# Kernel optimization log

Hardware: AMD Instinct MI355X
Metric: run time of the kernel (lower is better)

Reference implementation:

```python
import jax, jax.numpy as jnp
import numpy as np

B, D, N, H = 4, 1024, 2048, 16
HD = D // H  # head dim = 64


def rotate_half(x):
    # pairs (x1, x2) -> (-x2, x1), interleaved along last dim
    x1 = x[..., 0::2]
    x2 = x[..., 1::2]
    return jnp.stack((-x2, x1), axis=-1).reshape(x.shape)


def apply_cached_rotary_emb(freqs, t):
    return t * freqs[0] + rotate_half(t) * freqs[1]


def setup_inputs() -> dict:
    key = jax.random.key(0)
    ks = jax.random.split(key, 13)
    s = 1.0 / np.sqrt(D)
    inp = {
        "query": jax.random.normal(ks[0], (B, D, N), jnp.float32),
        "key": jax.random.normal(ks[1], (B, D, N), jnp.float32),
        "value": jax.random.normal(ks[2], (B, D, N), jnp.float32),
        "encoding": jax.random.normal(ks[3], (2, 1, 1, N, HD), jnp.float32),
        "Wq": jax.random.normal(ks[4], (D, D), jnp.float32) * s,
        "bq": jax.random.normal(ks[5], (D,), jnp.float32) * s,
        "Wk": jax.random.normal(ks[6], (D, D), jnp.float32) * s,
        "bk": jax.random.normal(ks[7], (D,), jnp.float32) * s,
        "Wv": jax.random.normal(ks[8], (D, D), jnp.float32) * s,
        "bv": jax.random.normal(ks[9], (D,), jnp.float32) * s,
        "Wm": jax.random.normal(ks[10], (D, D), jnp.float32) * s,
        "bm": jax.random.normal(ks[11], (D,), jnp.float32) * s,
    }
    return inp


def reference(query, key, value, encoding, Wq, bq, Wk, bk, Wv, bv, Wm, bm):
    b, d_model, n = query.shape

    def proj(W, bias, x):  # Conv1d with kernel_size=1 == pointwise matmul
        return jnp.einsum('oi,bin->bon', W, x) + bias[None, :, None]

    # [B, D, N] -> [B, HD, H, N]  (channel split: dim-major, as in .view(B, dim, H, -1))
    q = proj(Wq, bq, query).reshape(b, HD, H, n)
    k = proj(Wk, bk, key).reshape(b, HD, H, n)
    v = proj(Wv, bv, value).reshape(b, HD, H, n)

    # RoPE applied in [B, H, N, HD] layout, then back to [B, HD, H, N]
    q = jnp.transpose(apply_cached_rotary_emb(encoding, jnp.transpose(q, (0, 2, 3, 1))), (0, 3, 1, 2))
    k = jnp.transpose(apply_cached_rotary_emb(encoding, jnp.transpose(k, (0, 2, 3, 1))), (0, 3, 1, 2))

    scores = jnp.einsum('bdhn,bdhm->bhnm', q, k) / np.float32(np.sqrt(HD))
    prob = jax.nn.softmax(scores, axis=-1)
    x = jnp.einsum('bhnm,bdhm->bdhn', prob, v)

    out = jnp.einsum('oi,bin->bon', Wm, x.reshape(b, d_model, n)) + bm[None, :, None]
    return out
```

## Files before the change

kernel.cpp:

```cpp
#include <hip/hip_runtime.h>
#include <hip/hip_bf16.h>

typedef __bf16 bf16;
typedef __bf16 bf16x8 __attribute__((ext_vector_type(8)));
typedef __bf16 bf16x4 __attribute__((ext_vector_type(4)));
typedef float f32x4 __attribute__((ext_vector_type(4)));

#define LOG2E 1.44269504088896340736f

typedef __attribute__((address_space(1))) const unsigned int guint;
typedef __attribute__((address_space(3))) unsigned int luint;

__device__ __forceinline__ void gload_lds16(const bf16* g, bf16* l) {
  __builtin_amdgcn_global_load_lds((guint*)g, (luint*)l, 16, 0, 0);
}

__global__ __launch_bounds__(256) void k_transpose3(const float* __restrict__ q,
                                                    const float* __restrict__ k,
                                                    const float* __restrict__ v,
                                                    bf16* __restrict__ tq,
                                                    bf16* __restrict__ tk,
                                                    bf16* __restrict__ tv) {
  __shared__ bf16 T[64][72];
  const int t = threadIdx.x;
  const int n0 = blockIdx.x * 64;
  const int i0 = blockIdx.y * 64;
  const int z = blockIdx.z;
  const int b = z & 3, which = z >> 2;
  const float* src = (which == 0) ? q : ((which == 1) ? k : v);
  bf16* dst = (which == 0) ? tq : ((which == 1) ? tk : tv);
  const size_t srcb = (size_t)b * 1024 * 2048;
#pragma unroll
  for (int p = 0; p < 2; ++p) {
    int idx = p * 256 + t;
    int row = idx >> 3;
    int seg = idx & 7;
    const float* sp = src + srcb + (size_t)(i0 + row) * 2048 + n0 + seg * 8;
    f32x4 a = *(const f32x4*)sp;
    f32x4 c = *(const f32x4*)(sp + 4);
    bf16x8 o;
#pragma unroll
    for (int e = 0; e < 4; ++e) { o[e] = (bf16)a[e]; o[4 + e] = (bf16)c[e]; }
    *(bf16x8*)&T[row][seg * 8] = o;
  }
  __syncthreads();
  const int j = t >> 2;
  const int iseg = t & 3;
  bf16x8 o0, o1;
#pragma unroll
  for (int e = 0; e < 8; ++e) o0[e] = T[iseg * 16 + e][j];
#pragma unroll
  for (int e = 0; e < 8; ++e) o1[e] = T[iseg * 16 + 8 + e][j];
  bf16* dp = dst + (size_t)b * 2048 * 1024 + (size_t)(n0 + j) * 1024 + i0 + iseg * 16;
  *(bf16x8*)dp = o0;
  *(bf16x8*)(dp + 8) = o1;
}

__global__ __launch_bounds__(256) void k_gemm3(const bf16* __restrict__ Wqb,
                                               const bf16* __restrict__ Wkb,
                                               const bf16* __restrict__ Wvb,
                                               const float* __restrict__ bq,
                                               const float* __restrict__ bk,
                                               const float* __restrict__ bv,
                                               const bf16* __restrict__ tq,
                                               const bf16* __restrict__ tk,
                                               const bf16* __restrict__ tv,
                                               bf16* __restrict__ qp,
                                               bf16* __restrict__ kp,
                                               bf16* __restrict__ vp) {
  const int K = 1024, Nn = 2048;
  const int z = blockIdx.z;
  const int b = z & 3, which = z >> 2;
  const bf16* A = (which == 0) ? Wqb : ((which == 1) ? Wkb : Wvb);
  const bf16* Bt = (which == 0) ? tq : ((which == 1) ? tk : tv);
  const float* bias = (which == 0) ? bq : ((which == 1) ? bk : bv);
  bf16* C = (which == 0) ? qp : ((which == 1) ? kp : vp);

  __shared__ bf16 As[128 * 32];
  __shared__ bf16 Bs[128 * 32];
  const int t = threadIdx.x;
  const int w = t >> 6, l = t & 63, q = l >> 4, li = l & 15;
  const int o0 = blockIdx.y * 128, n0 = blockIdx.x * 128;
  const bf16* Ab = A + (size_t)o0 * K;
  const bf16* Bb = Bt + (size_t)b * Nn * K + (size_t)n0 * K;
  const int wr = (w >> 1) * 64, wc = (w & 1) * 64;
  f32x4 acc[4][4];
#pragma unroll
  for (int i = 0; i < 4; ++i)
#pragma unroll
    for (int j = 0; j < 4; ++j) acc[i][j] = (f32x4){0.f, 0.f, 0.f, 0.f};

  const int sidx0 = w * 64 + l;
  const int srow0 = sidx0 >> 2, sseg0 = (sidx0 & 3) * 8;
  const int sidx1 = 256 + sidx0;
  const int srow1 = sidx1 >> 2, sseg1 = (sidx1 & 3) * 8;
  bf16* ldsA0 = As + (size_t)(w * 64) * 8;
  bf16* ldsA1 = As + (size_t)(256 + w * 64) * 8;
  bf16* ldsB0 = Bs + (size_t)(w * 64) * 8;
  bf16* ldsB1 = Bs + (size_t)(256 + w * 64) * 8;

  for (int k0 = 0; k0 < K; k0 += 32) {
    __syncthreads();
    gload_lds16(Ab + (size_t)srow0 * K + k0 + sseg0, ldsA0);
    gload_lds16(Ab + (size_t)srow1 * K + k0 + sseg1, ldsA1);
    gload_lds16(Bb + (size_t)srow0 * K + k0 + sseg0, ldsB0);
    gload_lds16(Bb + (size_t)srow1 * K + k0 + sseg1, ldsB1);
    __syncthreads();
    bf16x8 af[4], bfr[4];
#pragma unroll
    for (int mt = 0; mt < 4; ++mt) af[mt] = *(const bf16x8*)&As[(wr + mt * 16 + li) * 32 + q * 8];
#pragma unroll
    for (int c = 0; c < 4; ++c) bfr[c] = *(const bf16x8*)&Bs[(wc + c * 16 + li) * 32 + q * 8];
#pragma unroll
    for (int mt = 0; mt < 4; ++mt)
#pragma unroll
      for (int c = 0; c < 4; ++c)
        acc[mt][c] = __builtin_amdgcn_mfma_f32_16x16x32_bf16(af[mt], bfr[c], acc[mt][c], 0, 0, 0);
  }

  bf16* Cb = C + (size_t)b * K * Nn;
#pragma unroll
  for (int mt = 0; mt < 4; ++mt) {
#pragma unroll
    for (int r = 0; r < 4; ++r) {
      int o = o0 + wr + mt * 16 + q * 4 + r;
      float bvv = bias[o];
#pragma unroll
      for (int c = 0; c < 4; ++c) {
        int n = n0 + wc + c * 16 + li;
        Cb[(size_t)o * Nn + n] = (bf16)(acc[mt][c][r] + bvv);
      }
    }
  }
}

template <typename OT>
__global__ __launch_bounds__(256) void k_gemm(const bf16* __restrict__ A,
                                              const bf16* __restrict__ Bt,
                                              const float* __restrict__ bias,
                                              OT* __restrict__ C,
                                              int M, int K, int Nn) {
  __shared__ bf16 As[128 * 32];
  __shared__ bf16 Bs[128 * 32];
  const int t = threadIdx.x;
  const int w = t >> 6, l = t & 63, q = l >> 4, li = l & 15;
  const int o0 = blockIdx.y * 128, n0 = blockIdx.x * 128;
  const int b = blockIdx.z;
  const bf16* Ab = A + (size_t)o0 * K;
  const bf16* Bb = Bt + (size_t)b * Nn * K + (size_t)n0 * K;
  const int wr = (w >> 1) * 64, wc = (w & 1) * 64;
  f32x4 acc[4][4];
#pragma unroll
  for (int i = 0; i < 4; ++i)
#pragma unroll
    for (int j = 0; j < 4; ++j) acc[i][j] = (f32x4){0.f, 0.f, 0.f, 0.f};

  const int sidx0 = w * 64 + l;
  const int srow0 = sidx0 >> 2, sseg0 = (sidx0 & 3) * 8;
  const int sidx1 = 256 + sidx0;
  const int srow1 = sidx1 >> 2, sseg1 = (sidx1 & 3) * 8;
  bf16* ldsA0 = As + (size_t)(w * 64) * 8;
  bf16* ldsA1 = As + (size_t)(256 + w * 64) * 8;
  bf16* ldsB0 = Bs + (size_t)(w * 64) * 8;
  bf16* ldsB1 = Bs + (size_t)(256 + w * 64) * 8;

  for (int k0 = 0; k0 < K; k0 += 32) {
    __syncthreads();
    gload_lds16(Ab + (size_t)srow0 * K + k0 + sseg0, ldsA0);
    gload_lds16(Ab + (size_t)srow1 * K + k0 + sseg1, ldsA1);
    gload_lds16(Bb + (size_t)srow0 * K + k0 + sseg0, ldsB0);
    gload_lds16(Bb + (size_t)srow1 * K + k0 + sseg1, ldsB1);
    __syncthreads();
    bf16x8 af[4], bfr[4];
#pragma unroll
    for (int mt = 0; mt < 4; ++mt) af[mt] = *(const bf16x8*)&As[(wr + mt * 16 + li) * 32 + q * 8];
#pragma unroll
    for (int c = 0; c < 4; ++c) bfr[c] = *(const bf16x8*)&Bs[(wc + c * 16 + li) * 32 + q * 8];
#pragma unroll
    for (int mt = 0; mt < 4; ++mt)
#pragma unroll
      for (int c = 0; c < 4; ++c)
        acc[mt][c] = __builtin_amdgcn_mfma_f32_16x16x32_bf16(af[mt], bfr[c], acc[mt][c], 0, 0, 0);
  }

  OT* Cb = C + (size_t)b * M * Nn;
#pragma unroll
  for (int mt = 0; mt < 4; ++mt) {
#pragma unroll
    for (int r = 0; r < 4; ++r) {
      int o = o0 + wr + mt * 16 + q * 4 + r;
      float bv = bias[o];
#pragma unroll
      for (int c = 0; c < 4; ++c) {
        int n = n0 + wc + c * 16 + li;
        Cb[(size_t)o * Nn + n] = (OT)(acc[mt][c][r] + bv);
      }
    }
  }
}

__global__ __launch_bounds__(256) void k_rope2(const bf16* __restrict__ qp,
                                               const bf16* __restrict__ kp,
                                               const float* __restrict__ enc,
                                               bf16* __restrict__ qa,
                                               bf16* __restrict__ ka) {
  __shared__ bf16 T[64][72];
  const int t = threadIdx.x;
  const int n0 = blockIdx.x * 64;
  const int h = blockIdx.y;
  const int z = blockIdx.z;
  const int b = z & 3, which = z >> 2;
  const bf16* src = which ? kp : qp;
  bf16* dst = which ? ka : qa;
  const float oscale = which ? 1.0f : 0.125f * LOG2E;
#pragma unroll
  for (int p = 0; p < 2; ++p) {
    int idx = p * 256 + t;
    int hd = idx >> 3;
    int seg = idx & 7;
    *(bf16x8*)&T[hd][seg * 8] =
        *(const bf16x8*)(src + (size_t)(b * 1024 + hd * 16 + h) * 2048 + n0 + seg * 8);
  }
  __syncthreads();
  const int j = t >> 2;
  const int hd0 = (t & 3) * 16;
  const int n = n0 + j;
  const float* e0 = enc + (size_t)n * 64 + hd0;
  const float* e1 = enc + (size_t)2048 * 64 + (size_t)n * 64 + hd0;
  bf16x8 o0, o1;
#pragma unroll
  for (int i = 0; i < 8; ++i) {
    int e = 2 * i;
    float t0 = (float)T[hd0 + e][j];
    float t1 = (float)T[hd0 + e + 1][j];
    float f00 = e0[e], f01 = e0[e + 1];
    float f10 = e1[e], f11 = e1[e + 1];
    float r0 = (t0 * f00 - t1 * f10) * oscale;
    float r1 = (t1 * f01 + t0 * f11) * oscale;
    if (i < 4) { o0[e & 7] = (bf16)r0; o0[(e & 7) + 1] = (bf16)r1; }
    else       { o1[e & 7] = (bf16)r0; o1[(e & 7) + 1] = (bf16)r1; }
  }
  bf16* dp = dst + ((size_t)(b * 16 + h) * 2048 + n) * 64 + hd0;
  *(bf16x8*)dp = o0;
  *(bf16x8*)(dp + 8) = o1;
}

__global__ __launch_bounds__(256, 4) void k_attn(const bf16* __restrict__ qa,
                                                 const bf16* __restrict__ ka,
                                                 const bf16* __restrict__ vp,
                                                 bf16* __restrict__ xo) {
  __shared__ bf16 Ks[64 * 72];
  __shared__ bf16 Vs[64 * 72];
  __shared__ bf16 Ps[4][32 * 72];
  const int t = threadIdx.x;
  const int w = t >> 6, l = t & 63, q = l >> 4, li = l & 15;
  const int n0 = blockIdx.x * 128, h = blockIdx.y, b = blockIdx.z;
  const bf16* Qb = qa + (size_t)(b * 16 + h) * 2048 * 64;
  const bf16* Kb = ka + (size_t)(b * 16 + h) * 2048 * 64;
  const bf16* Vb = vp + (size_t)b * 1024 * 2048 + (size_t)h * 2048;
  bf16* Pw = &Ps[w][0];

  const int r0 = t >> 3, s0 = (t & 7) * 8;
  const int r1 = (256 + t) >> 3, s1 = (t & 7) * 8;

  bf16x8 qf[2][2];
#pragma unroll
  for (int bt = 0; bt < 2; ++bt)
#pragma unroll
    for (int kk = 0; kk < 2; ++kk)
      qf[bt][kk] = *(const bf16x8*)(Qb + (size_t)(n0 + w * 32 + bt * 16 + li) * 64 + kk * 32 + q * 8);

  bf16x8 onef;
#pragma unroll
  for (int e = 0; e < 8; ++e) onef[e] = (bf16)1.0f;

  f32x4 acc[4][2];
#pragma unroll
  for (int i = 0; i < 4; ++i)
#pragma unroll
    for (int j = 0; j < 2; ++j) acc[i][j] = (f32x4){0.f, 0.f, 0.f, 0.f};
  f32x4 accl[2] = {(f32x4){0.f, 0.f, 0.f, 0.f}, (f32x4){0.f, 0.f, 0.f, 0.f}};

  bf16x8 kr0, kr1, vr0, vr1;
  kr0 = *(const bf16x8*)(Kb + (size_t)r0 * 64 + s0);
  kr1 = *(const bf16x8*)(Kb + (size_t)r1 * 64 + s1);
  vr0 = *(const bf16x8*)(Vb + (size_t)r0 * 32768 + s0);
  vr1 = *(const bf16x8*)(Vb + (size_t)r1 * 32768 + s1);
  *(bf16x8*)&Ks[r0 * 72 + s0] = kr0;
  *(bf16x8*)&Ks[r1 * 72 + s1] = kr1;
  *(bf16x8*)&Vs[r0 * 72 + s0] = vr0;
  *(bf16x8*)&Vs[r1 * 72 + s1] = vr1;
  __syncthreads();

  for (int m0 = 0; m0 < 2048; m0 += 64) {
    const int mn = (m0 + 64 < 2048) ? m0 + 64 : m0;
    kr0 = *(const bf16x8*)(Kb + (size_t)(mn + r0) * 64 + s0);
    kr1 = *(const bf16x8*)(Kb + (size_t)(mn + r1) * 64 + s1);
    vr0 = *(const bf16x8*)(Vb + (size_t)r0 * 32768 + mn + s0);
    vr1 = *(const bf16x8*)(Vb + (size_t)r1 * 32768 + mn + s1);

    f32x4 sacc[4][2];
#pragma unroll
    for (int mt = 0; mt < 4; ++mt)
#pragma unroll
      for (int bt = 0; bt < 2; ++bt) sacc[mt][bt] = (f32x4){0.f, 0.f, 0.f, 0.f};
#pragma unroll
    for (int kk = 0; kk < 2; ++kk) {
#pragma unroll
      for (int mt = 0; mt < 4; ++mt) {
        bf16x8 af = *(const bf16x8*)&Ks[(mt * 16 + li) * 72 + kk * 32 + q * 8];
#pragma unroll
        for (int bt = 0; bt < 2; ++bt)
          sacc[mt][bt] = __builtin_amdgcn_mfma_f32_16x16x32_bf16(af, qf[bt][kk], sacc[mt][bt], 0, 0, 0);
      }
    }

#pragma unroll
    for (int mt = 0; mt < 4; ++mt)
#pragma unroll
      for (int bt = 0; bt < 2; ++bt) {
        bf16x4 pk;
#pragma unroll
        for (int r = 0; r < 4; ++r) pk[r] = (bf16)__builtin_amdgcn_exp2f(sacc[mt][bt][r]);
        *(bf16x4*)&Pw[(bt * 16 + li) * 72 + mt * 16 + q * 4] = pk;
      }
    asm volatile("s_waitcnt lgkmcnt(0)" ::: "memory");

#pragma unroll
    for (int kk = 0; kk < 2; ++kk) {
      bf16x8 pf[2];
#pragma unroll
      for (int bt = 0; bt < 2; ++bt) {
        pf[bt] = *(const bf16x8*)&Pw[(bt * 16 + li) * 72 + kk * 32 + q * 8];
        accl[bt] = __builtin_amdgcn_mfma_f32_16x16x32_bf16(onef, pf[bt], accl[bt], 0, 0, 0);
      }
#pragma unroll
      for (int hdt = 0; hdt < 4; ++hdt) {
        bf16x8 vf = *(const bf16x8*)&Vs[(hdt * 16 + li) * 72 + kk * 32 + q * 8];
#pragma unroll
        for (int bt = 0; bt < 2; ++bt)
          acc[hdt][bt] = __builtin_amdgcn_mfma_f32_16x16x32_bf16(vf, pf[bt], acc[hdt][bt], 0, 0, 0);
      }
    }

    __syncthreads();
    *(bf16x8*)&Ks[r0 * 72 + s0] = kr0;
    *(bf16x8*)&Ks[r1 * 72 + s1] = kr1;
    *(bf16x8*)&Vs[r0 * 72 + s0] = vr0;
    *(bf16x8*)&Vs[r1 * 72 + s1] = vr1;
    __syncthreads();
  }

  float inv[2] = {1.0f / accl[0][0], 1.0f / accl[1][0]};

  bf16* xb = xo + (size_t)b * 2048 * 1024 + (size_t)h * 64;
#pragma unroll
  for (int hdt = 0; hdt < 4; ++hdt)
#pragma unroll
    for (int bt = 0; bt < 2; ++bt) {
      int n = n0 + w * 32 + bt * 16 + li;
      bf16x4 o;
#pragma unroll
      for (int r = 0; r < 4; ++r) o[r] = (bf16)(acc[hdt][bt][r] * inv[bt]);
      *(bf16x4*)(xb + (size_t)n * 1024 + hdt * 16 + q * 4) = o;
    }
}

__global__ __launch_bounds__(256) void k_prepw(const float* __restrict__ Wq,
                                               const float* __restrict__ Wk,
                                               const float* __restrict__ Wv,
                                               const float* __restrict__ Wm,
                                               bf16* __restrict__ oq,
                                               bf16* __restrict__ ok,
                                               bf16* __restrict__ ov,
                                               bf16* __restrict__ om) {
  const int which = blockIdx.y;
  if (which < 3) {
    const float* s = (which == 0) ? Wq : ((which == 1) ? Wk : Wv);
    bf16* d = (which == 0) ? oq : ((which == 1) ? ok : ov);
    int idx = (blockIdx.x * 256 + threadIdx.x) * 4;
    f32x4 a = *(const f32x4*)(s + idx);
    bf16x4 o;
#pragma unroll
    for (int e = 0; e < 4; ++e) o[e] = (bf16)a[e];
    *(bf16x4*)(d + idx) = o;
  } else {
#pragma unroll
    for (int p = 0; p < 4; ++p) {
      int idx = (blockIdx.x * 4 + p) * 256 + threadIdx.x;
      int o = idx >> 10, j = idx & 1023;
      int hd = j & 63, hh = j >> 6;
      om[idx] = (bf16)Wm[((size_t)o << 10) + (size_t)(hd * 16 + hh)];
    }
  }
}

extern "C" void kernel_launch(void* const* d_in, const int* in_sizes, int n_in,
                              void* d_out, int out_size, void* d_ws, size_t ws_size,
                              hipStream_t stream) {
  const float* query = (const float*)d_in[0];
  const float* key   = (const float*)d_in[1];
  const float* value = (const float*)d_in[2];
  const float* enc   = (const float*)d_in[3];
  const float* Wq = (const float*)d_in[4];  const float* bq = (const float*)d_in[5];
  const float* Wk = (const float*)d_in[6];  const float* bk = (const float*)d_in[7];
  const float* Wv = (const float*)d_in[8];  const float* bv = (const float*)d_in[9];
  const float* Wm = (const float*)d_in[10]; const float* bm = (const float*)d_in[11];

  char* ws = (char*)d_ws;
  const size_t SZ = (size_t)4 * 2048 * 1024 * 2;
  const size_t WZ = (size_t)1024 * 1024 * 2;
  bf16* bufA = (bf16*)(ws + 0 * SZ);
  bf16* bufB = (bf16*)(ws + 1 * SZ);
  bf16* bufC = (bf16*)(ws + 2 * SZ);
  bf16* bufD = (bf16*)(ws + 3 * SZ);
  bf16* Wqb  = (bf16*)(ws + 4 * SZ + 0 * WZ);
  bf16* Wkb  = (bf16*)(ws + 4 * SZ + 1 * WZ);
  bf16* Wvb  = (bf16*)(ws + 4 * SZ + 2 * WZ);
  bf16* Wmp  = (bf16*)(ws + 4 * SZ + 3 * WZ);
  bf16* vt   = (bf16*)d_out;
  bf16* vpd  = (bf16*)d_out + (size_t)4 * 2048 * 1024;

  dim3 blk(256);
  k_prepw<<<dim3(1024, 4), blk, 0, stream>>>(Wq, Wk, Wv, Wm, Wqb, Wkb, Wvb, Wmp);
  k_transpose3<<<dim3(32, 16, 12), blk, 0, stream>>>(query, key, value, bufA, bufB, vt);
  k_gemm3<<<dim3(16, 8, 12), blk, 0, stream>>>(Wqb, Wkb, Wvb, bq, bk, bv,
                                               bufA, bufB, vt, bufC, bufD, vpd);
  k_rope2<<<dim3(32, 16, 8), blk, 0, stream>>>(bufC, bufD, enc, bufA, bufB);
  k_attn<<<dim3(16, 16, 4), blk, 0, stream>>>(bufA, bufB, vpd, bufC);
  k_gemm<float><<<dim3(16, 8, 4), blk, 0, stream>>>(Wmp, bufC, bm, (float*)d_out, 1024, 1024, 2048);
}
```

Measured before the change: 368.3 us.

## Double-buffer attention K/V tiles, keep P in registers, swizzle transpose LDS

The attention kernel now double-buffers its K/V shared-memory tiles, which drops one barrier per 64-key step. It also rebuilds the P operand for the PV MFMA in registers using permlane32_swap and ds_swizzle, instead of writing P to shared memory and reading it back. The transpose and RoPE kernels XOR-swizzle their LDS tile columns to cut bank conflicts on the column-strided reads. The cost is more LDS for K/V, in-register shuffles that depend on the exact MFMA lane layout, and a correctness risk if the permute mapping is wrong.

After: 378.4 us. 2.7% more time.

```diff
diff --git a/kernel.cpp b/kernel.cpp
--- a/kernel.cpp
+++ b/kernel.cpp
@@ -5,6 +5,8 @@
 typedef __bf16 bf16x8 __attribute__((ext_vector_type(8)));
 typedef __bf16 bf16x4 __attribute__((ext_vector_type(4)));
 typedef float f32x4 __attribute__((ext_vector_type(4)));
+typedef unsigned int uint4v __attribute__((ext_vector_type(4)));
+typedef unsigned int uint2v __attribute__((ext_vector_type(2)));
 
 #define LOG2E 1.44269504088896340736f
 
@@ -35,22 +37,24 @@
     int idx = p * 256 + t;
     int row = idx >> 3;
     int seg = idx & 7;
+    int xm = (row >> 4) << 1;
     const float* sp = src + srcb + (size_t)(i0 + row) * 2048 + n0 + seg * 8;
     f32x4 a = *(const f32x4*)sp;
     f32x4 c = *(const f32x4*)(sp + 4);
     bf16x8 o;
 #pragma unroll
-    for (int e = 0; e < 4; ++e) { o[e] = (bf16)a[e]; o[4 + e] = (bf16)c[e]; }
+    for (int e = 0; e < 4; ++e) { o[e ^ xm] = (bf16)a[e]; o[(4 + e) ^ xm] = (bf16)c[e]; }
     *(bf16x8*)&T[row][seg * 8] = o;
   }
   __syncthreads();
   const int j = t >> 2;
   const int iseg = t & 3;
+  const int jx = j ^ (iseg << 1);
   bf16x8 o0, o1;
 #pragma unroll
-  for (int e = 0; e < 8; ++e) o0[e] = T[iseg * 16 + e][j];
-#pragma unroll
-  for (int e = 0; e < 8; ++e) o1[e] = T[iseg * 16 + 8 + e][j];
+  for (int e = 0; e < 8; ++e) o0[e] = T[iseg * 16 + e][jx];
+#pragma unroll
+  for (int e = 0; e < 8; ++e) o1[e] = T[iseg * 16 + 8 + e][jx];
   bf16* dp = dst + (size_t)b * 2048 * 1024 + (size_t)(n0 + j) * 1024 + i0 + iseg * 16;
   *(bf16x8*)dp = o0;
   *(bf16x8*)(dp + 8) = o1;
@@ -218,12 +222,17 @@
     int idx = p * 256 + t;
     int hd = idx >> 3;
     int seg = idx & 7;
-    *(bf16x8*)&T[hd][seg * 8] =
-        *(const bf16x8*)(src + (size_t)(b * 1024 + hd * 16 + h) * 2048 + n0 + seg * 8);
+    int xm = (hd >> 4) << 1;
+    bf16x8 v = *(const bf16x8*)(src + (size_t)(b * 1024 + hd * 16 + h) * 2048 + n0 + seg * 8);
+    bf16x8 o;
+#pragma unroll
+    for (int e = 0; e < 8; ++e) o[e ^ xm] = v[e];
+    *(bf16x8*)&T[hd][seg * 8] = o;
   }
   __syncthreads();
   const int j = t >> 2;
   const int hd0 = (t & 3) * 16;
+  const int jx = j ^ ((t & 3) << 1);
   const int n = n0 + j;
   const float* e0 = enc + (size_t)n * 64 + hd0;
   const float* e1 = enc + (size_t)2048 * 64 + (size_t)n * 64 + hd0;
@@ -231,8 +240,8 @@
 #pragma unroll
   for (int i = 0; i < 8; ++i) {
     int e = 2 * i;
-    float t0 = (float)T[hd0 + e][j];
-    float t1 = (float)T[hd0 + e + 1][j];
+    float t0 = (float)T[hd0 + e][jx];
+    float t1 = (float)T[hd0 + e + 1][jx];
     float f00 = e0[e], f01 = e0[e + 1];
     float f10 = e1[e], f11 = e1[e + 1];
     float r0 = (t0 * f00 - t1 * f10) * oscale;
@@ -245,20 +254,70 @@
   *(bf16x8*)(dp + 8) = o1;
 }
 
+#define ATTN_COMPUTE(KS, VS)                                                              \
+  {                                                                                       \
+    f32x4 sacc[4][2];                                                                     \
+    _Pragma("unroll") for (int mt = 0; mt < 4; ++mt)                                      \
+        _Pragma("unroll") for (int bt = 0; bt < 2; ++bt)                                  \
+            sacc[mt][bt] = (f32x4){0.f, 0.f, 0.f, 0.f};                                   \
+    _Pragma("unroll") for (int kk = 0; kk < 2; ++kk) {                                    \
+      _Pragma("unroll") for (int mt = 0; mt < 4; ++mt) {                                  \
+        bf16x8 af = *(const bf16x8*)&(KS)[(mt * 16 + li) * 72 + kk * 32 + q * 8];         \
+        _Pragma("unroll") for (int bt = 0; bt < 2; ++bt)                                  \
+            sacc[mt][bt] =                                                                \
+                __builtin_amdgcn_mfma_f32_16x16x32_bf16(af, qf[bt][kk], sacc[mt][bt], 0, 0, 0); \
+      }                                                                                   \
+    }                                                                                     \
+    unsigned pk32[2][4][2];                                                               \
+    _Pragma("unroll") for (int mt = 0; mt < 4; ++mt)                                      \
+        _Pragma("unroll") for (int bt = 0; bt < 2; ++bt) {                                \
+      bf16x4 pk;                                                                          \
+      _Pragma("unroll") for (int r = 0; r < 4; ++r)                                       \
+          pk[r] = (bf16)__builtin_amdgcn_exp2f(sacc[mt][bt][r]);                          \
+      uint2v pu = __builtin_bit_cast(uint2v, pk);                                         \
+      pk32[bt][mt][0] = pu[0];                                                            \
+      pk32[bt][mt][1] = pu[1];                                                            \
+    }                                                                                     \
+    _Pragma("unroll") for (int kk = 0; kk < 2; ++kk) {                                    \
+      bf16x8 pf[2];                                                                       \
+      _Pragma("unroll") for (int bt = 0; bt < 2; ++bt) {                                  \
+        uint4v du;                                                                        \
+        _Pragma("unroll") for (int hh = 0; hh < 2; ++hh) {                                \
+          unsigned p0 = pk32[bt][2 * kk + 0][hh];                                         \
+          unsigned p1 = pk32[bt][2 * kk + 1][hh];                                         \
+          uint2v ab = __builtin_amdgcn_permlane32_swap(p0, p1, false, false);             \
+          unsigned A = ab[0];                                                             \
+          unsigned Bv = ab[1];                                                            \
+          unsigned swzA = (unsigned)__builtin_amdgcn_ds_swizzle((int)A, 0x401F);          \
+          unsigned swzB = (unsigned)__builtin_amdgcn_ds_swizzle((int)Bv, 0x401F);         \
+          du[hh] = oddrow ? swzB : A;                                                     \
+          du[2 + hh] = oddrow ? Bv : swzA;                                                \
+        }                                                                                 \
+        pf[bt] = __builtin_bit_cast(bf16x8, du);                                          \
+        accl[bt] = __builtin_amdgcn_mfma_f32_16x16x32_bf16(onef, pf[bt], accl[bt], 0, 0, 0); \
+      }                                                                                   \
+      _Pragma("unroll") for (int hdt = 0; hdt < 4; ++hdt) {                               \
+        bf16x8 vf = *(const bf16x8*)&(VS)[(hdt * 16 + li) * 72 + kk * 32 + q * 8];        \
+        _Pragma("unroll") for (int bt = 0; bt < 2; ++bt)                                  \
+            acc[hdt][bt] =                                                                \
+                __builtin_amdgcn_mfma_f32_16x16x32_bf16(vf, pf[bt], acc[hdt][bt], 0, 0, 0); \
+      }                                                                                   \
+    }                                                                                     \
+  }
+
 __global__ __launch_bounds__(256, 4) void k_attn(const bf16* __restrict__ qa,
                                                  const bf16* __restrict__ ka,
                                                  const bf16* __restrict__ vp,
                                                  bf16* __restrict__ xo) {
-  __shared__ bf16 Ks[64 * 72];
-  __shared__ bf16 Vs[64 * 72];
-  __shared__ bf16 Ps[4][32 * 72];
+  __shared__ bf16 Ks2[2][64 * 72];
+  __shared__ bf16 Vs2[2][64 * 72];
   const int t = threadIdx.x;
   const int w = t >> 6, l = t & 63, q = l >> 4, li = l & 15;
   const int n0 = blockIdx.x * 128, h = blockIdx.y, b = blockIdx.z;
+  const bool oddrow = ((t >> 4) & 1) != 0;
   const bf16* Qb = qa + (size_t)(b * 16 + h) * 2048 * 64;
   const bf16* Kb = ka + (size_t)(b * 16 + h) * 2048 * 64;
   const bf16* Vb = vp + (size_t)b * 1024 * 2048 + (size_t)h * 2048;
-  bf16* Pw = &Ps[w][0];
 
   const int r0 = t >> 3, s0 = (t & 7) * 8;
   const int r1 = (256 + t) >> 3, s1 = (t & 7) * 8;
@@ -286,69 +345,40 @@
   kr1 = *(const bf16x8*)(Kb + (size_t)r1 * 64 + s1);
   vr0 = *(const bf16x8*)(Vb + (size_t)r0 * 32768 + s0);
   vr1 = *(const bf16x8*)(Vb + (size_t)r1 * 32768 + s1);
-  *(bf16x8*)&Ks[r0 * 72 + s0] = kr0;
-  *(bf16x8*)&Ks[r1 * 72 + s1] = kr1;
-  *(bf16x8*)&Vs[r0 * 72 + s0] = vr0;
-  *(bf16x8*)&Vs[r1 * 72 + s1] = vr1;
+  *(bf16x8*)&Ks2[0][r0 * 72 + s0] = kr0;
+  *(bf16x8*)&Ks2[0][r1 * 72 + s1] = kr1;
+  *(bf16x8*)&Vs2[0][r0 * 72 + s0] = vr0;
+  *(bf16x8*)&Vs2[0][r1 * 72 + s1] = vr1;
   __syncthreads();
 
-  for (int m0 = 0; m0 < 2048; m0 += 64) {
-    const int mn = (m0 + 64 < 2048) ? m0 + 64 : m0;
-    kr0 = *(const bf16x8*)(Kb + (size_t)(mn + r0) * 64 + s0);
-    kr1 = *(const bf16x8*)(Kb + (size_t)(mn + r1) * 64 + s1);
-    vr0 = *(const bf16x8*)(Vb + (size_t)r0 * 32768 + mn + s0);
-    vr1 = *(const bf16x8*)(Vb + (size_t)r1 * 32768 + mn + s1);
-
-    f32x4 sacc[4][2];
-#pragma unroll
-    for (int mt = 0; mt < 4; ++mt)
-#pragma unroll
-      for (int bt = 0; bt < 2; ++bt) sacc[mt][bt] = (f32x4){0.f, 0.f, 0.f, 0.f};
-#pragma unroll
-    for (int kk = 0; kk < 2; ++kk) {
-#pragma unroll
-      for (int mt = 0; mt < 4; ++mt) {
-        bf16x8 af = *(const bf16x8*)&Ks[(mt * 16 + li) * 72 + kk * 32 + q * 8];
-#pragma unroll
-        for (int bt = 0; bt < 2; ++bt)
-          sacc[mt][bt] = __builtin_amdgcn_mfma_f32_16x16x32_bf16(af, qf[bt][kk], sacc[mt][bt], 0, 0, 0);
-      }
-    }
-
-#pragma unroll
-    for (int mt = 0; mt < 4; ++mt)
-#pragma unroll
-      for (int bt = 0; bt < 2; ++bt) {
-        bf16x4 pk;
-#pragma unroll
-        for (int r = 0; r < 4; ++r) pk[r] = (bf16)__builtin_amdgcn_exp2f(sacc[mt][bt][r]);
-        *(bf16x4*)&Pw[(bt * 16 + li) * 72 + mt * 16 + q * 4] = pk;
-      }
-    asm volatile("s_waitcnt lgkmcnt(0)" ::: "memory");
-
-#pragma unroll
-    for (int kk = 0; kk < 2; ++kk) {
-      bf16x8 pf[2];
-#pragma unroll
-      for (int bt = 0; bt < 2; ++bt) {
-        pf[bt] = *(const bf16x8*)&Pw[(bt * 16 + li) * 72 + kk * 32 + q * 8];
-        accl[bt] = __builtin_amdgcn_mfma_f32_16x16x32_bf16(onef, pf[bt], accl[bt], 0, 0, 0);
-      }
-#pragma unroll
-      for (int hdt = 0; hdt < 4; ++hdt) {
-        bf16x8 vf = *(const bf16x8*)&Vs[(hdt * 16 + li) * 72 + kk * 32 + q * 8];
-#pragma unroll
-        for (int bt = 0; bt < 2; ++bt)
-          acc[hdt][bt] = __builtin_amdgcn_mfma_f32_16x16x32_bf16(vf, pf[bt], acc[hdt][bt], 0, 0, 0);
-      }
-    }
-
-    __syncthreads();
-    *(bf16x8*)&Ks[r0 * 72 + s0] = kr0;
-    *(bf16x8*)&Ks[r1 * 72 + s1] = kr1;
-    *(bf16x8*)&Vs[r0 * 72 + s0] = vr0;
-    *(bf16x8*)&Vs[r1 * 72 + s1] = vr1;
-    __syncthreads();
+#pragma unroll 1
+  for (int m0 = 0; m0 < 2048; m0 += 128) {
+    {
+      const int mn = m0 + 64;
+      kr0 = *(const bf16x8*)(Kb + (size_t)(mn + r0) * 64 + s0);
+      kr1 = *(const bf16x8*)(Kb + (size_t)(mn + r1) * 64 + s1);
+      vr0 = *(const bf16x8*)(Vb + (size_t)r0 * 32768 + mn + s0);
+      vr1 = *(const bf16x8*)(Vb + (size_t)r1 * 32768 + mn + s1);
+      ATTN_COMPUTE(Ks2[0], Vs2[0])
+      *(bf16x8*)&Ks2[1][r0 * 72 + s0] = kr0;
+      *(bf16x8*)&Ks2[1][r1 * 72 + s1] = kr1;
+      *(bf16x8*)&Vs2[1][r0 * 72 + s0] = vr0;
+      *(bf16x8*)&Vs2[1][r1 * 72 + s1] = vr1;
+      __syncthreads();
+    }
+    {
+      const int mn = (m0 + 128 < 2048) ? m0 + 128 : 0;
+      kr0 = *(const bf16x8*)(Kb + (size_t)(mn + r0) * 64 + s0);
+      kr1 = *(const bf16x8*)(Kb + (size_t)(mn + r1) * 64 + s1);
+      vr0 = *(const bf16x8*)(Vb + (size_t)r0 * 32768 + mn + s0);
+      vr1 = *(const bf16x8*)(Vb + (size_t)r1 * 32768 + mn + s1);
+      ATTN_COMPUTE(Ks2[1], Vs2[1])
+      *(bf16x8*)&Ks2[0][r0 * 72 + s0] = kr0;
+      *(bf16x8*)&Ks2[0][r1 * 72 + s1] = kr1;
+      *(bf16x8*)&Vs2[0][r0 * 72 + s0] = vr0;
+      *(bf16x8*)&Vs2[0][r1 * 72 + s1] = vr1;
+      __syncthreads();
+    }
   }
 
   float inv[2] = {1.0f / accl[0][0], 1.0f / accl[1][0]};
```
